# Kernel tuning notes

Hardware: AMD Instinct MI355X
Metric: run time of the kernel (lower is better)

Reference implementation:

```python
import jax, jax.numpy as jnp
import numpy as np

GRAPH_BIAS_SCALE = 0.7
COMMITMENT_COST = 0.25
DECAY = 0.995
EPS = 1e-6

N_TOKENS = 32768
LATENT = 512
N_SYMBOLS = 8192
EMBED_DIM = 2 * LATENT


def setup_inputs() -> dict:
    key = jax.random.key(0)
    ks = jax.random.split(key, 6)
    return {
        "z_real": jax.random.normal(ks[0], (N_TOKENS, LATENT), jnp.float32),
        "z_imag": jax.random.normal(ks[1], (N_TOKENS, LATENT), jnp.float32),
        "prev_symbol_idx": jax.random.randint(ks[2], (N_TOKENS,), 0, N_SYMBOLS, jnp.int64),
        "codebook": jax.random.normal(ks[3], (N_SYMBOLS, EMBED_DIM), jnp.float32),
        "cluster_size": jax.random.uniform(ks[4], (N_SYMBOLS,), jnp.float32),
        "embed_avg": jax.random.normal(ks[5], (N_SYMBOLS, EMBED_DIM), jnp.float32),
        "adjacency": jax.random.normal(jax.random.fold_in(key, 7), (N_SYMBOLS, N_SYMBOLS), jnp.float32),
    }


def reference(z_real, z_imag, prev_symbol_idx, codebook, cluster_size, embed_avg, adjacency):
    n_symbols = codebook.shape[0]
    z_flat = jnp.concatenate([z_real, z_imag], axis=-1)  # [N, 2*latent]

    # squared-distance matrix via matmul expansion: [N, n_symbols]
    d = (jnp.sum(z_flat ** 2, axis=1, keepdims=True)
         + jnp.sum(codebook ** 2, axis=1)
         - 2.0 * z_flat @ codebook.T)

    # graph-adjacency prior bias (row gather + sigmoid)
    bias = GRAPH_BIAS_SCALE * jax.nn.sigmoid(adjacency[prev_symbol_idx])
    d = d - bias

    min_indices = jnp.argmin(d, axis=1)          # [N]
    z_q = codebook[min_indices]                  # gather, pre-EMA codebook

    # --- EMA codebook update (training mode), scatter via segment_sum ---
    ones = jnp.ones(min_indices.shape, jnp.float32)
    counts = jax.ops.segment_sum(ones, min_indices, num_segments=n_symbols)
    new_cluster_size = cluster_size * DECAY + counts * (1.0 - DECAY)
    embed_sum = jax.ops.segment_sum(jax.lax.stop_gradient(z_flat), min_indices,
                                    num_segments=n_symbols)
    new_embed_avg = embed_avg * DECAY + embed_sum * (1.0 - DECAY)
    n_total = jnp.sum(new_cluster_size)
    cs = (new_cluster_size + EPS) / (n_total + n_symbols * EPS) * n_total
    new_codebook = new_embed_avg / cs[:, None]

    # --- losses and straight-through estimator ---
    loss_vq = jnp.mean((z_q - jax.lax.stop_gradient(z_flat)) ** 2)
    loss_commit = jnp.mean((jax.lax.stop_gradient(z_q) - z_flat) ** 2)
    loss = loss_vq + COMMITMENT_COST * loss_commit

    z_q_st = z_flat + jax.lax.stop_gradient(z_q - z_flat)
    D = z_real.shape[-1]
    z_complex = jax.lax.complex(z_q_st[..., :D], z_q_st[..., D:])

    return z_complex, loss, min_indices, new_codebook, new_cluster_size, new_embed_avg
```

## Files before the change

kernel.cpp:

```cpp
#include <hip/hip_runtime.h>
#include <math.h>
#include <float.h>

#define M_TOK   32768
#define NSYM    8192
#define KDIM    1024
#define LAT     512

#define DECAY_F 0.995f
#define OMD_F   0.005f
#define GBS_F   0.7f
#define EPS_F   1e-6f
#define WIN_F   2.5f

typedef unsigned short u16;
typedef unsigned int   u32;
typedef short short8 __attribute__((ext_vector_type(8)));
typedef float f32x4  __attribute__((ext_vector_type(4)));

#define GLOAD_LDS16(g, l) \
    __builtin_amdgcn_global_load_lds((const __attribute__((address_space(1))) u32*)(g), \
                                     (__attribute__((address_space(3))) u32*)(l), 16, 0, 0)

__device__ __forceinline__ u16 f2bf(float f) {
    u32 u = __float_as_uint(f);
    return (u16)((u + 0x7FFF + ((u >> 16) & 1)) >> 16);
}

__global__ void k_convA(const float* __restrict__ zr, const float* __restrict__ zi,
                        u16* __restrict__ A) {
    size_t t = (size_t)blockIdx.x * 256 + threadIdx.x;
    size_t base = t * 8;
    int tok = (int)(base >> 10);
    int k0  = (int)(base & 1023);
    const float* src = (k0 < 512) ? zr + (size_t)tok * 512 + k0
                                  : zi + (size_t)tok * 512 + (k0 - 512);
    float4 f0 = *(const float4*)src;
    float4 f1 = *(const float4*)(src + 4);
    u32 q0 = f2bf(f0.x) | ((u32)f2bf(f0.y) << 16);
    u32 q1 = f2bf(f0.z) | ((u32)f2bf(f0.w) << 16);
    u32 q2 = f2bf(f1.x) | ((u32)f2bf(f1.y) << 16);
    u32 q3 = f2bf(f1.z) | ((u32)f2bf(f1.w) << 16);
    *(uint4*)&A[base] = make_uint4(q0, q1, q2, q3);
}

__global__ void k_convB(const float* __restrict__ cb, u16* __restrict__ B,
                        float* __restrict__ cnorm) {
    size_t t = (size_t)blockIdx.x * 256 + threadIdx.x;
    size_t base = t * 8;
    float4 f0 = *(const float4*)&cb[base];
    float4 f1 = *(const float4*)&cb[base + 4];
    u32 q0 = f2bf(f0.x) | ((u32)f2bf(f0.y) << 16);
    u32 q1 = f2bf(f0.z) | ((u32)f2bf(f0.w) << 16);
    u32 q2 = f2bf(f1.x) | ((u32)f2bf(f1.y) << 16);
    u32 q3 = f2bf(f1.z) | ((u32)f2bf(f1.w) << 16);
    *(uint4*)&B[base] = make_uint4(q0, q1, q2, q3);
    float nrm = f0.x * f0.x + f0.y * f0.y + f0.z * f0.z + f0.w * f0.w
              + f1.x * f1.x + f1.y * f1.y + f1.z * f1.z + f1.w * f1.w;
#pragma unroll
    for (int m = 32; m; m >>= 1) nrm += __shfl_xor(nrm, m, 64);
    __shared__ float part[4];
    int lane = threadIdx.x & 63, w = threadIdx.x >> 6;
    if (lane == 0) part[w] = nrm;
    __syncthreads();
    if (threadIdx.x == 0)   cnorm[blockIdx.x * 2]     = part[0] + part[1];
    if (threadIdx.x == 128) cnorm[blockIdx.x * 2 + 1] = part[2] + part[3];
}

__global__ __launch_bounds__(256, 4) void k_screen(
    const u16* __restrict__ Ah, const u16* __restrict__ Bh,
    const float* __restrict__ cnorm,
    float* __restrict__ candV, u16* __restrict__ candI)
{
    __shared__ __align__(16) unsigned char smA[16384];
    __shared__ __align__(16) unsigned char smB[16384];
    __shared__ float smv[128][2][2];
    __shared__ float smi[128][2];

    const int sblk = (blockIdx.x & 7) * 128 + (blockIdx.x >> 3);
    const int bx = sblk >> 2;
    const int by = sblk & 3;

    const int tid  = threadIdx.x;
    const int lane = tid & 63;
    const int w    = tid >> 6;
    const int wr   = w >> 1, wc = w & 1;
    const int row0 = bx * 128;
    const int sBase = w * 256;

    for (int cc = 0; cc < 16; ++cc) {
        const int chunk = by * 16 + cc;
        const int colBase = chunk * 128;

        f32x4 acc[4][4];
#pragma unroll
        for (int m = 0; m < 4; ++m)
#pragma unroll
            for (int n = 0; n < 4; ++n) acc[m][n] = (f32x4){0.f, 0.f, 0.f, 0.f};

        for (int ks = 0; ks < 16; ++ks) {
            const int kk0 = ks * 64;
            __syncthreads();
#pragma unroll
            for (int i = 0; i < 4; ++i) {
                int slot = sBase + i * 64 + lane;
                int r = slot >> 3;
                int c = (slot & 7) ^ (r & 7);
                const u16* ga = Ah + ((size_t)(row0 + r) * KDIM + kk0 + c * 8);
                GLOAD_LDS16(ga, smA + (size_t)(sBase + i * 64) * 16);
                const u16* gb = Bh + ((size_t)(colBase + r) * KDIM + kk0 + c * 8);
                GLOAD_LDS16(gb, smB + (size_t)(sBase + i * 64) * 16);
            }
            __syncthreads();
#pragma unroll
            for (int h = 0; h < 2; ++h) {
                short8 af[4], bfr[4];
#pragma unroll
                for (int m = 0; m < 4; ++m) {
                    int r = wr * 64 + m * 16 + (lane & 15);
                    int byte = r * 128 + h * 64 + (lane >> 4) * 16;
                    byte ^= (r & 7) << 4;
                    af[m] = *(const short8*)(smA + byte);
                }
#pragma unroll
                for (int n = 0; n < 4; ++n) {
                    int r = wc * 64 + n * 16 + (lane & 15);
                    int byte = r * 128 + h * 64 + (lane >> 4) * 16;
                    byte ^= (r & 7) << 4;
                    bfr[n] = *(const short8*)(smB + byte);
                }
#pragma unroll
                for (int m = 0; m < 4; ++m)
#pragma unroll
                    for (int n = 0; n < 4; ++n)
                        acc[m][n] = __builtin_amdgcn_mfma_f32_16x16x32_bf16(
                            af[m], bfr[n], acc[m][n], 0, 0, 0);
            }
        }

        float cn[4];
#pragma unroll
        for (int n = 0; n < 4; ++n)
            cn[n] = cnorm[colBase + wc * 64 + n * 16 + (lane & 15)];

#pragma unroll
        for (int m = 0; m < 4; ++m)
#pragma unroll
            for (int j = 0; j < 4; ++j) {
                int rowL = wr * 64 + m * 16 + (lane >> 4) * 4 + j;
                float v1 = INFINITY, v2 = INFINITY, i1v = 0.f;
#pragma unroll
                for (int n = 0; n < 4; ++n) {
                    float s = cn[n] - 2.0f * acc[m][n][j];
                    float ci = (float)(colBase + wc * 64 + n * 16 + (lane & 15));
                    if (s < v1) { v2 = v1; v1 = s; i1v = ci; }
                    else v2 = fminf(v2, s);
                }
#pragma unroll
                for (int msk = 1; msk < 16; msk <<= 1) {
                    float o1 = __shfl_xor(v1, msk, 16);
                    float oi = __shfl_xor(i1v, msk, 16);
                    float o2 = __shfl_xor(v2, msk, 16);
                    float n2 = fminf(fminf(v2, o2), fmaxf(v1, o1));
                    if (o1 < v1) { v1 = o1; i1v = oi; }
                    v2 = n2;
                }
                if ((lane & 15) == 0) {
                    smv[rowL][wc][0] = v1;  smv[rowL][wc][1] = v2;
                    smi[rowL][wc] = i1v;
                }
            }
        __syncthreads();
        {
            int half = tid >> 7;
            int row  = tid & 127;
            float v1 = smv[row][half][0], v2 = smv[row][half][1];
            float iv = smi[row][half];
            size_t tcol = (size_t)(row0 + row);
            int halfIdx = chunk * 2 + half;
            candV[(size_t)(halfIdx * 2 + 0) * M_TOK + tcol] = v1;
            candV[(size_t)(halfIdx * 2 + 1) * M_TOK + tcol] = v2;
            candI[(size_t)halfIdx * M_TOK + tcol]           = (u16)iv;
        }
    }
}

__global__ void k_zero(u32* __restrict__ counts, u32* __restrict__ cursors,
                       u32* __restrict__ qcount, float* __restrict__ out_loss) {
    int i = blockIdx.x * 256 + threadIdx.x;
    if (i < NSYM) { counts[i] = 0; cursors[i] = 0; }
    if (i == 0) { out_loss[0] = 0.0f; qcount[0] = 0; }
}

__device__ __forceinline__ void rescore(
    const float* __restrict__ codebook, const float* __restrict__ adjacency,
    const double* zreg, int prw, int col, int lane, double& bestS, int& bestI)
{
    const float* crow = codebook + (size_t)col * KDIM;
    double dot = 0.0, cn2 = 0.0;
#pragma unroll
    for (int j = 0; j < 16; ++j) {
        double c = (double)crow[lane + 64 * j];
        dot += c * zreg[j]; cn2 += c * c;
    }
#pragma unroll
    for (int m = 32; m; m >>= 1) {
        dot += __shfl_xor(dot, m, 64);
        cn2 += __shfl_xor(cn2, m, 64);
    }
    double a = (double)adjacency[(size_t)prw * NSYM + col];
    double sc = cn2 - 2.0 * dot - (double)GBS_F / (1.0 + exp(-a));
    if (sc < bestS || (sc == bestS && col < bestI)) { bestS = sc; bestI = col; }
}

#define SEL_TOK 32
__global__ __launch_bounds__(256) void k_select(
    const float* __restrict__ zr, const float* __restrict__ zi,
    const int* __restrict__ prev,
    const float* __restrict__ codebook,
    const float* __restrict__ adjacency,
    const float* __restrict__ candV, const u16* __restrict__ candI,
    float* __restrict__ out_idx, u32* __restrict__ counts,
    u32* __restrict__ qcount, u32* __restrict__ queue)
{
    __shared__ float sv[256][SEL_TOK + 1];
    __shared__ u16   si[128][SEL_TOK + 2];
    const int tok0 = blockIdx.x * SEL_TOK;
    const int w = threadIdx.x >> 6, lane = threadIdx.x & 63;

    for (int idx = threadIdx.x; idx < 256 * SEL_TOK; idx += 256) {
        int e = idx >> 5, t = idx & (SEL_TOK - 1);
        sv[e][t] = candV[(size_t)e * M_TOK + tok0 + t];
    }
    for (int idx = threadIdx.x; idx < 128 * SEL_TOK; idx += 256) {
        int e = idx >> 5, t = idx & (SEL_TOK - 1);
        si[e][t] = candI[(size_t)e * M_TOK + tok0 + t];
    }
    __syncthreads();

    for (int tt = 0; tt < SEL_TOK / 4; ++tt) {
        const int t = w * (SEL_TOK / 4) + tt;
        const int tok = tok0 + t;
        float va1 = sv[4 * lane + 0][t];
        float va2 = sv[4 * lane + 1][t];
        float vb1 = sv[4 * lane + 2][t];
        float vb2 = sv[4 * lane + 3][t];
        int   ia  = (int)si[2 * lane + 0][t];
        int   ib  = (int)si[2 * lane + 1][t];

        float mm = fminf(va1, vb1);
#pragma unroll
        for (int m = 32; m; m >>= 1) mm = fminf(mm, __shfl_xor(mm, m, 64));
        const float thr = mm + WIN_F;

        unsigned long long m1a = __ballot(va1 <= thr);
        unsigned long long m1b = __ballot(vb1 <= thr);
        unsigned long long mh  = __ballot(va2 <= thr) | __ballot(vb2 <= thr);

        if (mh != 0) {
            if (lane == 0) { u32 q = atomicAdd(qcount, 1u); queue[q] = (u32)tok; }
        } else if (__popcll(m1a) + __popcll(m1b) == 1) {
            int bestI;
            if (m1a) { int c = __ffsll(m1a) - 1; bestI = __shfl(ia, c, 64); }
            else     { int c = __ffsll(m1b) - 1; bestI = __shfl(ib, c, 64); }
            if (lane == 0) {
                out_idx[tok] = (float)bestI;
                atomicAdd(&counts[bestI], 1u);
            }
        } else {
            double zreg[16];
#pragma unroll
            for (int j = 0; j < 8; ++j)
                zreg[j] = (double)zr[(size_t)tok * LAT + lane + 64 * j];
#pragma unroll
            for (int j = 0; j < 8; ++j)
                zreg[8 + j] = (double)zi[(size_t)tok * LAT + lane + 64 * j];
            const int prw = prev[tok];
            double bestS = DBL_MAX; int bestI = 0x7FFFFFFF;
            unsigned long long sa = m1a, sb = m1b;
            while (sa) { int c = __ffsll(sa) - 1; sa &= sa - 1;
                rescore(codebook, adjacency, zreg, prw, __shfl(ia, c, 64), lane, bestS, bestI); }
            while (sb) { int c = __ffsll(sb) - 1; sb &= sb - 1;
                rescore(codebook, adjacency, zreg, prw, __shfl(ib, c, 64), lane, bestS, bestI); }
            if (lane == 0) {
                out_idx[tok] = (float)bestI;
                atomicAdd(&counts[bestI], 1u);
            }
        }
    }
}

#define MAXC 384
__global__ __launch_bounds__(256) void k_rescan(
    const float* __restrict__ zr, const float* __restrict__ zi,
    const int* __restrict__ prev,
    const float* __restrict__ codebook,
    const float* __restrict__ adjacency,
    const float* __restrict__ candV, const u16* __restrict__ candI,
    const u32* __restrict__ qcount, const u32* __restrict__ queue,
    float* __restrict__ out_idx, u32* __restrict__ counts)
{
    __shared__ double zd[KDIM];
    __shared__ float v1h[128], v2h[128];
    __shared__ u16   i1h[128];
    __shared__ int   collist[MAXC];
    __shared__ int   nsing_sh, nh_sh, scanall_sh;
    __shared__ int   halves[128];
    __shared__ double wsc[4];
    __shared__ int    wix[4];
    __shared__ float  mm_sh;

    const int tid = threadIdx.x;
    const int w = tid >> 6, lane = tid & 63;
    const u32 nq = qcount[0];

    for (u32 qi = blockIdx.x; qi < nq; qi += gridDim.x) {
        const int tok = (int)queue[qi];

        if (tid < 128) {
            v1h[tid] = candV[(size_t)(tid * 2 + 0) * M_TOK + tok];
            v2h[tid] = candV[(size_t)(tid * 2 + 1) * M_TOK + tok];
            i1h[tid] = candI[(size_t)tid * M_TOK + tok];
        }
        for (int k = tid; k < LAT; k += 256) {
            zd[k]       = (double)zr[(size_t)tok * LAT + k];
            zd[LAT + k] = (double)zi[(size_t)tok * LAT + k];
        }
        if (tid == 0) { nsing_sh = 0; nh_sh = 0; scanall_sh = 0; }
        __syncthreads();

        if (tid < 64) {
            float m = fminf(v1h[tid], v1h[tid + 64]);
#pragma unroll
            for (int s = 32; s; s >>= 1) m = fminf(m, __shfl_xor(m, s, 64));
            if (tid == 0) mm_sh = m;
        }
        __syncthreads();
        const float thr = mm_sh + WIN_F;

        if (tid < 128) {
            bool hs = (v2h[tid] <= thr);
            if (hs) { int p = atomicAdd(&nh_sh, 1); halves[p] = tid; }
            else if (v1h[tid] <= thr) { int p = atomicAdd(&nsing_sh, 1); collist[p] = (int)i1h[tid]; }
        }
        __syncthreads();
        int nsing = nsing_sh, nh = nh_sh;
        int nc = nsing + nh * 64;
        if (nc > MAXC) { if (tid == 0) scanall_sh = 1; }
        __syncthreads();
        if (!scanall_sh) {
            for (int h = 0; h < nh; ++h) {
                if (tid < 64) collist[nsing + h * 64 + tid] = halves[h] * 64 + tid;
            }
            nc = nsing + nh * 64;
        }
        __syncthreads();

        const int prw = prev[tok];
        double bestS = DBL_MAX; int bestI = 0x7FFFFFFF;
        const int total = scanall_sh ? NSYM : nc;
        for (int ci = w; ci < total; ci += 4) {
            int col = scanall_sh ? ci : collist[ci];
            const float* crow = codebook + (size_t)col * KDIM;
            double dot = 0.0, cn2 = 0.0;
#pragma unroll
            for (int j = 0; j < 16; ++j) {
                double c = (double)crow[lane + 64 * j];
                dot += c * zd[lane + 64 * j]; cn2 += c * c;
            }
#pragma unroll
            for (int s = 32; s; s >>= 1) {
                dot += __shfl_xor(dot, s, 64);
                cn2 += __shfl_xor(cn2, s, 64);
            }
            double a = (double)adjacency[(size_t)prw * NSYM + col];
            double sc = cn2 - 2.0 * dot - (double)GBS_F / (1.0 + exp(-a));
            if (sc < bestS || (sc == bestS && col < bestI)) { bestS = sc; bestI = col; }
        }
        if (lane == 0) { wsc[w] = bestS; wix[w] = bestI; }
        __syncthreads();
        if (tid == 0) {
            double bs = wsc[0]; int bi = wix[0];
#pragma unroll
            for (int q = 1; q < 4; ++q) {
                if (wsc[q] < bs || (wsc[q] == bs && wix[q] < bi)) { bs = wsc[q]; bi = wix[q]; }
            }
            out_idx[tok] = (float)bi;
            atomicAdd(&counts[bi], 1u);
        }
        __syncthreads();
    }
}

__global__ __launch_bounds__(1024) void k_scan(
    const u32* __restrict__ counts, const float* __restrict__ cs_old,
    float* __restrict__ out_cs, u32* __restrict__ offsets,
    float* __restrict__ scal)
{
    const int tid = threadIdx.x;
    const int lane = tid & 63, w = tid >> 6;
    const int base = tid * 8;
    u32 c[8], pre[8], T = 0;
#pragma unroll
    for (int q = 0; q < 8; ++q) { c[q] = counts[base + q]; pre[q] = T; T += c[q]; }
    u32 inc = T;
#pragma unroll
    for (int d = 1; d < 64; d <<= 1) {
        u32 v = __shfl_up(inc, d, 64);
        if (lane >= d) inc += v;
    }
    __shared__ u32 wt[16];
    if (lane == 63) wt[w] = inc;
    __syncthreads();
    if (tid < 16) {
        u32 v = wt[tid];
#pragma unroll
        for (int d = 1; d < 16; d <<= 1) {
            u32 o = __shfl_up(v, d, 16);
            if (tid >= d) v += o;
        }
        wt[tid] = v;
    }
    __syncthreads();
    u32 ex = (w ? wt[w - 1] : 0) + inc - T;
#pragma unroll
    for (int q = 0; q < 8; ++q) offsets[base + q] = ex + pre[q];

    float nt = 0.0f;
#pragma unroll
    for (int q = 0; q < 8; ++q) {
        float ncs = cs_old[base + q] * DECAY_F + OMD_F * (float)c[q];
        out_cs[base + q] = ncs;
        nt += ncs;
    }
#pragma unroll
    for (int m = 32; m; m >>= 1) nt += __shfl_xor(nt, m, 64);
    __shared__ float red[16];
    if (lane == 0) red[w] = nt;
    __syncthreads();
    if (tid == 0) {
        float s = 0.0f;
#pragma unroll
        for (int i = 0; i < 16; ++i) s += red[i];
        scal[0] = s;
        scal[1] = s + (float)NSYM * EPS_F;
    }
}

__global__ void k_place(const float* __restrict__ idxf, const u32* __restrict__ offsets,
                        u32* __restrict__ cursors, u32* __restrict__ list) {
    int t = blockIdx.x * 256 + threadIdx.x;
    int s = (int)idxf[t];
    u32 slot = atomicAdd(&cursors[s], 1u);
    list[offsets[s] + slot] = (u32)t;
}

__global__ __launch_bounds__(128) void k_emit_fused(
    const float* __restrict__ zr, const float* __restrict__ zi,
    const float* __restrict__ codebook, const float* __restrict__ embed_avg,
    const u32* __restrict__ counts, const u32* __restrict__ offsets,
    const u32* __restrict__ list, const float* __restrict__ out_cs,
    const float* __restrict__ scal,
    float* __restrict__ out_ea, float* __restrict__ out_cb,
    float* __restrict__ out_zc, float* __restrict__ out_loss, int interleaved)
{
    const int s = blockIdx.x;
    const u32 cnt = counts[s], off = offsets[s];
    const int j = threadIdx.x * 4;
    float4 cbr = *(const float4*)&codebook[(size_t)s * KDIM + j];
    float4 cbi = *(const float4*)&codebook[(size_t)s * KDIM + LAT + j];
    float ar0 = 0.f, ar1 = 0.f, ar2 = 0.f, ar3 = 0.f;
    float ai0 = 0.f, ai1 = 0.f, ai2 = 0.f, ai3 = 0.f;
    float lsum = 0.f;
    for (u32 n = 0; n < cnt; ++n) {
        int t = (int)list[off + n];
        float4 z0 = *(const float4*)&zr[(size_t)t * LAT + j];
        float4 z1 = *(const float4*)&zi[(size_t)t * LAT + j];
        ar0 += z0.x; ar1 += z0.y; ar2 += z0.z; ar3 += z0.w;
        ai0 += z1.x; ai1 += z1.y; ai2 += z1.z; ai3 += z1.w;
        if (interleaved) {
            float2* dst = (float2*)out_zc + (size_t)t * LAT + j;
            dst[0] = make_float2(cbr.x, cbi.x); dst[1] = make_float2(cbr.y, cbi.y);
            dst[2] = make_float2(cbr.z, cbi.z); dst[3] = make_float2(cbr.w, cbi.w);
        } else {
            *(float4*)&out_zc[(size_t)t * LAT + j] = cbr;
        }
        float d;
        d = cbr.x - z0.x; lsum += d * d;  d = cbr.y - z0.y; lsum += d * d;
        d = cbr.z - z0.z; lsum += d * d;  d = cbr.w - z0.w; lsum += d * d;
        d = cbi.x - z1.x; lsum += d * d;  d = cbi.y - z1.y; lsum += d * d;
        d = cbi.z - z1.z; lsum += d * d;  d = cbi.w - z1.w; lsum += d * d;
    }
    float4 ea0 = *(const float4*)&embed_avg[(size_t)s * KDIM + j];
    float4 ea1 = *(const float4*)&embed_avg[(size_t)s * KDIM + LAT + j];
    float4 ner = make_float4(ea0.x * DECAY_F + ar0 * OMD_F, ea0.y * DECAY_F + ar1 * OMD_F,
                             ea0.z * DECAY_F + ar2 * OMD_F, ea0.w * DECAY_F + ar3 * OMD_F);
    float4 nei = make_float4(ea1.x * DECAY_F + ai0 * OMD_F, ea1.y * DECAY_F + ai1 * OMD_F,
                             ea1.z * DECAY_F + ai2 * OMD_F, ea1.w * DECAY_F + ai3 * OMD_F);
    *(float4*)&out_ea[(size_t)s * KDIM + j]       = ner;
    *(float4*)&out_ea[(size_t)s * KDIM + LAT + j] = nei;
    float ntot = scal[0], denom = scal[1];
    float cs = (out_cs[s] + EPS_F) / denom * ntot;
    float inv = 1.0f / cs;
    *(float4*)&out_cb[(size_t)s * KDIM + j] =
        make_float4(ner.x * inv, ner.y * inv, ner.z * inv, ner.w * inv);
    *(float4*)&out_cb[(size_t)s * KDIM + LAT + j] =
        make_float4(nei.x * inv, nei.y * inv, nei.z * inv, nei.w * inv);
#pragma unroll
    for (int m = 32; m; m >>= 1) lsum += __shfl_xor(lsum, m, 64);
    __shared__ float red[2];
    int wv = threadIdx.x >> 6, lane = threadIdx.x & 63;
    if (lane == 0) red[wv] = lsum;
    __syncthreads();
    if (threadIdx.x == 0) atomicAdd(out_loss, red[0] + red[1]);
}

__global__ __launch_bounds__(256) void k_emit(
    const float* __restrict__ zr, const float* __restrict__ zi,
    const float* __restrict__ embed_avg,
    const u32* __restrict__ counts, const u32* __restrict__ offsets,
    const u32* __restrict__ list, const float* __restrict__ out_cs,
    const float* __restrict__ scal,
    float* __restrict__ out_ea, float* __restrict__ out_cb)
{
    const int s = blockIdx.x;
    const u32 cnt = counts[s], off = offsets[s];
    const int j = threadIdx.x * 4;
    float a0 = 0.f, a1 = 0.f, a2 = 0.f, a3 = 0.f;
    for (u32 n = 0; n < cnt; ++n) {
        int t = (int)list[off + n];
        const float* src = (j < 512) ? zr + (size_t)t * 512 + j
                                     : zi + (size_t)t * 512 + (j - 512);
        float4 v = *(const float4*)src;
        a0 += v.x; a1 += v.y; a2 += v.z; a3 += v.w;
    }
    float4 ea = *(const float4*)&embed_avg[(size_t)s * KDIM + j];
    float4 nea = make_float4(ea.x * DECAY_F + a0 * OMD_F,
                             ea.y * DECAY_F + a1 * OMD_F,
                             ea.z * DECAY_F + a2 * OMD_F,
                             ea.w * DECAY_F + a3 * OMD_F);
    *(float4*)&out_ea[(size_t)s * KDIM + j] = nea;
    float ntot = scal[0], denom = scal[1];
    float cs = (out_cs[s] + EPS_F) / denom * ntot;
    float inv = 1.0f / cs;
    *(float4*)&out_cb[(size_t)s * KDIM + j] =
        make_float4(nea.x * inv, nea.y * inv, nea.z * inv, nea.w * inv);
}

__global__ __launch_bounds__(256) void k_zq(
    const float* __restrict__ zr, const float* __restrict__ zi,
    const float* __restrict__ codebook, const float* __restrict__ idxf,
    float* __restrict__ out_zc, float* __restrict__ out_loss, int interleaved)
{
    const int w = threadIdx.x >> 6, lane = threadIdx.x & 63;
    const int tok = blockIdx.x * 4 + w;
    const int mi = (int)idxf[tok];
    const int j0 = lane * 8;
    float4 re0 = *(const float4*)&codebook[(size_t)mi * KDIM + j0];
    float4 re1 = *(const float4*)&codebook[(size_t)mi * KDIM + j0 + 4];
    float4 im0 = *(const float4*)&codebook[(size_t)mi * KDIM + LAT + j0];
    float4 im1 = *(const float4*)&codebook[(size_t)mi * KDIM + LAT + j0 + 4];
    float4 zr0 = *(const float4*)&zr[(size_t)tok * LAT + j0];
    float4 zr1 = *(const float4*)&zr[(size_t)tok * LAT + j0 + 4];
    float4 zi0 = *(const float4*)&zi[(size_t)tok * LAT + j0];
    float4 zi1 = *(const float4*)&zi[(size_t)tok * LAT + j0 + 4];
    if (interleaved) {
        float2* dst = (float2*)out_zc + (size_t)tok * LAT + j0;
        dst[0] = make_float2(re0.x, im0.x); dst[1] = make_float2(re0.y, im0.y);
        dst[2] = make_float2(re0.z, im0.z); dst[3] = make_float2(re0.w, im0.w);
        dst[4] = make_float2(re1.x, im1.x); dst[5] = make_float2(re1.y, im1.y);
        dst[6] = make_float2(re1.z, im1.z); dst[7] = make_float2(re1.w, im1.w);
    } else {
        *(float4*)&out_zc[(size_t)tok * LAT + j0]     = re0;
        *(float4*)&out_zc[(size_t)tok * LAT + j0 + 4] = re1;
    }
    float l = 0.f;
    l += (re0.x-zr0.x)*(re0.x-zr0.x) + (re0.y-zr0.y)*(re0.y-zr0.y)
       + (re0.z-zr0.z)*(re0.z-zr0.z) + (re0.w-zr0.w)*(re0.w-zr0.w);
    l += (re1.x-zr1.x)*(re1.x-zr1.x) + (re1.y-zr1.y)*(re1.y-zr1.y)
       + (re1.z-zr1.z)*(re1.z-zr1.z) + (re1.w-zr1.w)*(re1.w-zr1.w);
    l += (im0.x-zi0.x)*(im0.x-zi0.x) + (im0.y-zi0.y)*(im0.y-zi0.y)
       + (im0.z-zi0.z)*(im0.z-zi0.z) + (im0.w-zi0.w)*(im0.w-zi0.w);
    l += (im1.x-zi1.x)*(im1.x-zi1.x) + (im1.y-zi1.y)*(im1.y-zi1.y)
       + (im1.z-zi1.z)*(im1.z-zi1.z) + (im1.w-zi1.w)*(im1.w-zi1.w);
#pragma unroll
    for (int m = 32; m; m >>= 1) l += __shfl_xor(l, m, 64);
    if (lane == 0) atomicAdd(out_loss, l);
}

__global__ void k_fin(float* __restrict__ out_loss) {
    out_loss[0] = out_loss[0] * 1.25f / 33554432.0f;
}

extern "C" void kernel_launch(void* const* d_in, const int* in_sizes, int n_in,
                              void* d_out, int out_size, void* d_ws, size_t ws_size,
                              hipStream_t stream) {
    const float* z_real     = (const float*)d_in[0];
    const float* z_imag     = (const float*)d_in[1];
    const int*   prev_idx   = (const int*)d_in[2];
    const float* codebook   = (const float*)d_in[3];
    const float* cluster_sz = (const float*)d_in[4];
    const float* embed_avg  = (const float*)d_in[5];
    const float* adjacency  = (const float*)d_in[6];

    float* out = (float*)d_out;

    const size_t REST = 1 + (size_t)M_TOK + (size_t)NSYM * KDIM + NSYM
                      + (size_t)NSYM * KDIM;
    size_t zc_n = (size_t)out_size - REST;
    const size_t n_z = (size_t)M_TOK * LAT;
    int interleaved = (zc_n >= 2 * n_z) ? 1 : 0;

    float* out_zc   = out;
    float* out_loss = out + zc_n;
    float* out_idx  = out + zc_n + 1;
    float* out_cb   = out + zc_n + 1 + M_TOK;
    float* out_cs   = out_cb + (size_t)NSYM * KDIM;
    float* out_ea   = out_cs + NSYM;

    u16*   A_hi  = (u16*)out_zc;
    u16*   B_hi  = (u16*)out_cb;
    float* cnorm = out_cb + 4194304;
    float* candV = out_ea;
    u16*   candI = (u16*)(out_cb + 4202496);

    const size_t WS_NEED = (size_t)(NSYM * 3 + M_TOK * 2 + 8) * 4;
    int use_ws = (ws_size >= WS_NEED) ? 1 : 0;
    u32 *counts, *cursors, *offsets, *list, *qcount, *queue;
    float* scal;
    if (use_ws) {
        u32* wsp = (u32*)d_ws;
        counts  = wsp;             cursors = counts + NSYM;
        offsets = cursors + NSYM;  list    = offsets + NSYM;
        queue   = list + M_TOK;
        scal    = (float*)(queue + M_TOK);
        qcount  = (u32*)(scal + 2);
    } else {
        counts  = (u32*)out_zc;    cursors = counts + NSYM;
        offsets = cursors + NSYM;  list    = offsets + NSYM;
        scal    = (float*)(list + M_TOK);
        qcount  = (u32*)(scal + 2);
        queue   = qcount + 1;
    }

    if (use_ws)
        k_zero<<<32, 256, 0, stream>>>(counts, cursors, qcount, out_loss);
    k_convA<<<16384, 256, 0, stream>>>(z_real, z_imag, A_hi);
    k_convB<<<4096, 256, 0, stream>>>(codebook, B_hi, cnorm);
    k_screen<<<1024, 256, 0, stream>>>(A_hi, B_hi, cnorm, candV, candI);
    if (!use_ws)
        k_zero<<<32, 256, 0, stream>>>(counts, cursors, qcount, out_loss);
    k_select<<<M_TOK / SEL_TOK, 256, 0, stream>>>(z_real, z_imag, prev_idx,
                                                  codebook, adjacency,
                                                  candV, candI, out_idx, counts,
                                                  qcount, queue);
    k_rescan<<<1024, 256, 0, stream>>>(z_real, z_imag, prev_idx, codebook,
                                       adjacency, candV, candI,
                                       qcount, queue, out_idx, counts);
    k_scan<<<1, 1024, 0, stream>>>(counts, cluster_sz, out_cs, offsets, scal);
    k_place<<<M_TOK / 256, 256, 0, stream>>>(out_idx, offsets, cursors, list);
    if (use_ws) {
        k_emit_fused<<<NSYM, 128, 0, stream>>>(z_real, z_imag, codebook, embed_avg,
                                               counts, offsets, list, out_cs, scal,
                                               out_ea, out_cb, out_zc, out_loss,
                                               interleaved);
    } else {
        k_emit<<<NSYM, 256, 0, stream>>>(z_real, z_imag, embed_avg, counts, offsets,
                                         list, out_cs, scal, out_ea, out_cb);
        k_zq<<<M_TOK / 4, 256, 0, stream>>>(z_real, z_imag, codebook, out_idx,
                                            out_zc, out_loss, interleaved);
    }
    k_fin<<<1, 1, 0, stream>>>(out_loss);
}
```

Measured before the change: 1.248 ms.

## Merge conversion and zeroing kernels, fuse scan with placement, drop final loss kernel

Merges the two bf16 conversion kernels and the zeroing kernel into one launch. Fuses the prefix scan with token placement in a single block that uses LDS atomics instead of global cursors, and folds the loss scaling into the atomic adds so the final one-thread kernel goes away. It also halves the tokens per select block and reduces the rescan grid. The aim is fewer launches and less global atomic traffic, at the cost of serialising 32K placements inside one workgroup.

```diff
diff --git a/kernel.cpp b/kernel.cpp
--- a/kernel.cpp
+++ b/kernel.cpp
@@ -12,6 +12,7 @@
 #define GBS_F   0.7f
 #define EPS_F   1e-6f
 #define WIN_F   2.5f
+#define LOSS_SCALE (1.25f / 33554432.0f)
 
 typedef unsigned short u16;
 typedef unsigned int   u32;
@@ -27,44 +28,53 @@
     return (u16)((u + 0x7FFF + ((u >> 16) & 1)) >> 16);
 }
 
-__global__ void k_convA(const float* __restrict__ zr, const float* __restrict__ zi,
-                        u16* __restrict__ A) {
-    size_t t = (size_t)blockIdx.x * 256 + threadIdx.x;
-    size_t base = t * 8;
-    int tok = (int)(base >> 10);
-    int k0  = (int)(base & 1023);
-    const float* src = (k0 < 512) ? zr + (size_t)tok * 512 + k0
-                                  : zi + (size_t)tok * 512 + (k0 - 512);
-    float4 f0 = *(const float4*)src;
-    float4 f1 = *(const float4*)(src + 4);
-    u32 q0 = f2bf(f0.x) | ((u32)f2bf(f0.y) << 16);
-    u32 q1 = f2bf(f0.z) | ((u32)f2bf(f0.w) << 16);
-    u32 q2 = f2bf(f1.x) | ((u32)f2bf(f1.y) << 16);
-    u32 q3 = f2bf(f1.z) | ((u32)f2bf(f1.w) << 16);
-    *(uint4*)&A[base] = make_uint4(q0, q1, q2, q3);
-}
-
-__global__ void k_convB(const float* __restrict__ cb, u16* __restrict__ B,
-                        float* __restrict__ cnorm) {
-    size_t t = (size_t)blockIdx.x * 256 + threadIdx.x;
-    size_t base = t * 8;
-    float4 f0 = *(const float4*)&cb[base];
-    float4 f1 = *(const float4*)&cb[base + 4];
-    u32 q0 = f2bf(f0.x) | ((u32)f2bf(f0.y) << 16);
-    u32 q1 = f2bf(f0.z) | ((u32)f2bf(f0.w) << 16);
-    u32 q2 = f2bf(f1.x) | ((u32)f2bf(f1.y) << 16);
-    u32 q3 = f2bf(f1.z) | ((u32)f2bf(f1.w) << 16);
-    *(uint4*)&B[base] = make_uint4(q0, q1, q2, q3);
-    float nrm = f0.x * f0.x + f0.y * f0.y + f0.z * f0.z + f0.w * f0.w
-              + f1.x * f1.x + f1.y * f1.y + f1.z * f1.z + f1.w * f1.w;
-#pragma unroll
-    for (int m = 32; m; m >>= 1) nrm += __shfl_xor(nrm, m, 64);
-    __shared__ float part[4];
-    int lane = threadIdx.x & 63, w = threadIdx.x >> 6;
-    if (lane == 0) part[w] = nrm;
-    __syncthreads();
-    if (threadIdx.x == 0)   cnorm[blockIdx.x * 2]     = part[0] + part[1];
-    if (threadIdx.x == 128) cnorm[blockIdx.x * 2 + 1] = part[2] + part[3];
+__global__ void k_conv(const float* __restrict__ zr, const float* __restrict__ zi,
+                       const float* __restrict__ cb,
+                       u16* __restrict__ A, u16* __restrict__ B,
+                       float* __restrict__ cnorm,
+                       u32* __restrict__ counts, u32* __restrict__ qcount,
+                       float* __restrict__ out_loss) {
+    const int bid = blockIdx.x;
+    if (bid < 16384) {
+        size_t t = (size_t)bid * 256 + threadIdx.x;
+        size_t base = t * 8;
+        int tok = (int)(base >> 10);
+        int k0  = (int)(base & 1023);
+        const float* src = (k0 < 512) ? zr + (size_t)tok * 512 + k0
+                                      : zi + (size_t)tok * 512 + (k0 - 512);
+        float4 f0 = *(const float4*)src;
+        float4 f1 = *(const float4*)(src + 4);
+        u32 q0 = f2bf(f0.x) | ((u32)f2bf(f0.y) << 16);
+        u32 q1 = f2bf(f0.z) | ((u32)f2bf(f0.w) << 16);
+        u32 q2 = f2bf(f1.x) | ((u32)f2bf(f1.y) << 16);
+        u32 q3 = f2bf(f1.z) | ((u32)f2bf(f1.w) << 16);
+        *(uint4*)&A[base] = make_uint4(q0, q1, q2, q3);
+    } else if (bid < 20480) {
+        const int b2 = bid - 16384;
+        size_t t = (size_t)b2 * 256 + threadIdx.x;
+        size_t base = t * 8;
+        float4 f0 = *(const float4*)&cb[base];
+        float4 f1 = *(const float4*)&cb[base + 4];
+        u32 q0 = f2bf(f0.x) | ((u32)f2bf(f0.y) << 16);
+        u32 q1 = f2bf(f0.z) | ((u32)f2bf(f0.w) << 16);
+        u32 q2 = f2bf(f1.x) | ((u32)f2bf(f1.y) << 16);
+        u32 q3 = f2bf(f1.z) | ((u32)f2bf(f1.w) << 16);
+        *(uint4*)&B[base] = make_uint4(q0, q1, q2, q3);
+        float nrm = f0.x * f0.x + f0.y * f0.y + f0.z * f0.z + f0.w * f0.w
+                  + f1.x * f1.x + f1.y * f1.y + f1.z * f1.z + f1.w * f1.w;
+#pragma unroll
+        for (int m = 32; m; m >>= 1) nrm += __shfl_xor(nrm, m, 64);
+        __shared__ float part[4];
+        int lane = threadIdx.x & 63, w = threadIdx.x >> 6;
+        if (lane == 0) part[w] = nrm;
+        __syncthreads();
+        if (threadIdx.x == 0)   cnorm[b2 * 2]     = part[0] + part[1];
+        if (threadIdx.x == 128) cnorm[b2 * 2 + 1] = part[2] + part[3];
+    } else {
+        int i = (bid - 20480) * 256 + threadIdx.x;
+        if (i < NSYM) counts[i] = 0;
+        if (i == 0) { qcount[0] = 0; out_loss[0] = 0.0f; }
+    }
 }
 
 __global__ __launch_bounds__(256, 4) void k_screen(
@@ -185,10 +195,10 @@
     }
 }
 
-__global__ void k_zero(u32* __restrict__ counts, u32* __restrict__ cursors,
-                       u32* __restrict__ qcount, float* __restrict__ out_loss) {
+__global__ void k_zero(u32* __restrict__ counts, u32* __restrict__ qcount,
+                       float* __restrict__ out_loss) {
     int i = blockIdx.x * 256 + threadIdx.x;
-    if (i < NSYM) { counts[i] = 0; cursors[i] = 0; }
+    if (i < NSYM) counts[i] = 0;
     if (i == 0) { out_loss[0] = 0.0f; qcount[0] = 0; }
 }
 
@@ -213,7 +223,7 @@
     if (sc < bestS || (sc == bestS && col < bestI)) { bestS = sc; bestI = col; }
 }
 
-#define SEL_TOK 32
+#define SEL_TOK 16
 __global__ __launch_bounds__(256) void k_select(
     const float* __restrict__ zr, const float* __restrict__ zi,
     const int* __restrict__ prev,
@@ -229,11 +239,11 @@
     const int w = threadIdx.x >> 6, lane = threadIdx.x & 63;
 
     for (int idx = threadIdx.x; idx < 256 * SEL_TOK; idx += 256) {
-        int e = idx >> 5, t = idx & (SEL_TOK - 1);
+        int e = idx >> 4, t = idx & (SEL_TOK - 1);
         sv[e][t] = candV[(size_t)e * M_TOK + tok0 + t];
     }
     for (int idx = threadIdx.x; idx < 128 * SEL_TOK; idx += 256) {
-        int e = idx >> 5, t = idx & (SEL_TOK - 1);
+        int e = idx >> 4, t = idx & (SEL_TOK - 1);
         si[e][t] = candI[(size_t)e * M_TOK + tok0 + t];
     }
     __syncthreads();
@@ -392,11 +402,15 @@
     }
 }
 
-__global__ __launch_bounds__(1024) void k_scan(
+__global__ __launch_bounds__(1024) void k_scanplace(
     const u32* __restrict__ counts, const float* __restrict__ cs_old,
+    const float* __restrict__ idxf,
     float* __restrict__ out_cs, u32* __restrict__ offsets,
-    float* __restrict__ scal)
-{
+    float* __restrict__ scal, u32* __restrict__ list)
+{
+    __shared__ u32 cur[NSYM];
+    __shared__ u32 wt[16];
+    __shared__ float red[16];
     const int tid = threadIdx.x;
     const int lane = tid & 63, w = tid >> 6;
     const int base = tid * 8;
@@ -409,7 +423,6 @@
         u32 v = __shfl_up(inc, d, 64);
         if (lane >= d) inc += v;
     }
-    __shared__ u32 wt[16];
     if (lane == 63) wt[w] = inc;
     __syncthreads();
     if (tid < 16) {
@@ -424,7 +437,10 @@
     __syncthreads();
     u32 ex = (w ? wt[w - 1] : 0) + inc - T;
 #pragma unroll
-    for (int q = 0; q < 8; ++q) offsets[base + q] = ex + pre[q];
+    for (int q = 0; q < 8; ++q) {
+        offsets[base + q] = ex + pre[q];
+        cur[base + q]     = ex + pre[q];
+    }
 
     float nt = 0.0f;
 #pragma unroll
@@ -435,7 +451,6 @@
     }
 #pragma unroll
     for (int m = 32; m; m >>= 1) nt += __shfl_xor(nt, m, 64);
-    __shared__ float red[16];
     if (lane == 0) red[w] = nt;
     __syncthreads();
     if (tid == 0) {
@@ -445,14 +460,13 @@
         scal[0] = s;
         scal[1] = s + (float)NSYM * EPS_F;
     }
-}
-
-__global__ void k_place(const float* __restrict__ idxf, const u32* __restrict__ offsets,
-                        u32* __restrict__ cursors, u32* __restrict__ list) {
-    int t = blockIdx.x * 256 + threadIdx.x;
-    int s = (int)idxf[t];
-    u32 slot = atomicAdd(&cursors[s], 1u);
-    list[offsets[s] + slot] = (u32)t;
+    __syncthreads();
+
+    for (int t = tid; t < M_TOK; t += 1024) {
+        int s = (int)idxf[t];
+        u32 slot = atomicAdd(&cur[s], 1u);
+        list[slot] = (u32)t;
+    }
 }
 
 __global__ __launch_bounds__(128) void k_emit_fused(
@@ -512,7 +526,7 @@
     int wv = threadIdx.x >> 6, lane = threadIdx.x & 63;
     if (lane == 0) red[wv] = lsum;
     __syncthreads();
-    if (threadIdx.x == 0) atomicAdd(out_loss, red[0] + red[1]);
+    if (threadIdx.x == 0) atomicAdd(out_loss, (red[0] + red[1]) * LOSS_SCALE);
 }
 
 __global__ __launch_bounds__(256) void k_emit(
@@ -585,11 +599,7 @@
        + (im1.z-zi1.z)*(im1.z-zi1.z) + (im1.w-zi1.w)*(im1.w-zi1.w);
 #pragma unroll
     for (int m = 32; m; m >>= 1) l += __shfl_xor(l, m, 64);
-    if (lane == 0) atomicAdd(out_loss, l);
-}
-
-__global__ void k_fin(float* __restrict__ out_loss) {
-    out_loss[0] = out_loss[0] * 1.25f / 33554432.0f;
+    if (lane == 0) atomicAdd(out_loss, l * LOSS_SCALE);
 }
 
 extern "C" void kernel_launch(void* const* d_in, const int* in_sizes, int n_in,
@@ -624,41 +634,39 @@
     float* candV = out_ea;
     u16*   candI = (u16*)(out_cb + 4202496);
 
-    const size_t WS_NEED = (size_t)(NSYM * 3 + M_TOK * 2 + 8) * 4;
+    const size_t WS_NEED = (size_t)(NSYM * 2 + M_TOK * 2 + 8) * 4;
     int use_ws = (ws_size >= WS_NEED) ? 1 : 0;
-    u32 *counts, *cursors, *offsets, *list, *qcount, *queue;
+    u32 *counts, *offsets, *list, *qcount, *queue;
     float* scal;
     if (use_ws) {
         u32* wsp = (u32*)d_ws;
-        counts  = wsp;             cursors = counts + NSYM;
-        offsets = cursors + NSYM;  list    = offsets + NSYM;
-        queue   = list + M_TOK;
+        counts  = wsp;             offsets = counts + NSYM;
+        list    = offsets + NSYM;  queue   = list + M_TOK;
         scal    = (float*)(queue + M_TOK);
         qcount  = (u32*)(scal + 2);
     } else {
-        counts  = (u32*)out_zc;    cursors = counts + NSYM;
-        offsets = cursors + NSYM;  list    = offsets + NSYM;
+        counts  = (u32*)out_zc;    offsets = counts + NSYM;
+        list    = offsets + NSYM;
         scal    = (float*)(list + M_TOK);
         qcount  = (u32*)(scal + 2);
         queue   = qcount + 1;
     }
 
-    if (use_ws)
-        k_zero<<<32, 256, 0, stream>>>(counts, cursors, qcount, out_loss);
-    k_convA<<<16384, 256, 0, stream>>>(z_real, z_imag, A_hi);
-    k_convB<<<4096, 256, 0, stream>>>(codebook, B_hi, cnorm);
+    k_conv<<<use_ws ? 20512 : 20480, 256, 0, stream>>>(z_real, z_imag, codebook,
+                                                       A_hi, B_hi, cnorm,
+                                                       counts, qcount, out_loss);
     k_screen<<<1024, 256, 0, stream>>>(A_hi, B_hi, cnorm, candV, candI);
     if (!use_ws)
-        k_zero<<<32, 256, 0, stream>>>(counts, cursors, qcount, out_loss);
+        k_zero<<<32, 256, 0, stream>>>(counts, qcount, out_loss);
     k_select<<<M_TOK / SEL_TOK, 256, 0, stream>>>(z_real, z_imag, prev_idx,
                                                   codebook, adjacency,
                                                   candV, candI, out_idx, counts,
                                                   qcount, queue);
-    k_rescan<<<1024, 256, 0, stream>>>(z_real, z_imag, prev_idx, codebook,
-                                       adjacency, candV, candI,
-                                       qcount, queue, out_idx, counts);
-    k_scan<<<1, 1024, 0, stream>>>(counts, cluster_sz, out_cs, offsets, scal);
-    k_place<<<M_TOK / 256, 256, 0, stream>>>(out_idx, offsets, cursors, list);
+    k_rescan<<<256, 256, 0, stream>>>(z_real, z_imag, prev_idx, codebook,
+                                      adjacency, candV, candI,
+                                      qcount, queue, out_idx, counts);
+    k_scanplace<<<1, 1024, 0, stream>>>(counts, cluster_sz, out_idx,
+                                        out_cs, offsets, scal, list);
     if (use_ws) {
         k_emit_fused<<<NSYM, 128, 0, stream>>>(z_real, z_imag, codebook, embed_avg,
                                                counts, offsets, list, out_cs, scal,
@@ -670,5 +678,4 @@
         k_zq<<<M_TOK / 4, 256, 0, stream>>>(z_real, z_imag, codebook, out_idx,
                                             out_zc, out_loss, interleaved);
     }
-    k_fin<<<1, 1, 0, stream>>>(out_loss);
-}
+}
```

Result: slower. 1.290 ms (+3.3%).

## Merge conversion and zeroing kernels, drop final loss kernel, widen EMA emit blocks

Applied to the files above, without the earlier changes.

Merges the A and B bf16 conversion kernels and the workspace zeroing into a single launch. The loss normalisation is folded into the per-block atomic adds, so the single-thread finalize kernel goes away. The fused EMA emit kernel now uses 256 threads, with two groups splitting each symbol's token list and combining partial sums through shared memory. The rescan grid shrinks from 1024 to 256 blocks, and the screening GEMM is split into two half-grid launches using a block offset. The aim is to cut launch overhead and add parallelism in the emit stage, at the cost of an extra launch for the screen and more float rounding in the loss from per-block scaling.

```diff
diff --git a/kernel.cpp b/kernel.cpp
--- a/kernel.cpp
+++ b/kernel.cpp
@@ -12,6 +12,7 @@
 #define GBS_F   0.7f
 #define EPS_F   1e-6f
 #define WIN_F   2.5f
+#define LOSS_SCALE (1.25f / 33554432.0f)
 
 typedef unsigned short u16;
 typedef unsigned int   u32;
@@ -27,57 +28,67 @@
     return (u16)((u + 0x7FFF + ((u >> 16) & 1)) >> 16);
 }
 
-__global__ void k_convA(const float* __restrict__ zr, const float* __restrict__ zi,
-                        u16* __restrict__ A) {
-    size_t t = (size_t)blockIdx.x * 256 + threadIdx.x;
-    size_t base = t * 8;
-    int tok = (int)(base >> 10);
-    int k0  = (int)(base & 1023);
-    const float* src = (k0 < 512) ? zr + (size_t)tok * 512 + k0
-                                  : zi + (size_t)tok * 512 + (k0 - 512);
-    float4 f0 = *(const float4*)src;
-    float4 f1 = *(const float4*)(src + 4);
-    u32 q0 = f2bf(f0.x) | ((u32)f2bf(f0.y) << 16);
-    u32 q1 = f2bf(f0.z) | ((u32)f2bf(f0.w) << 16);
-    u32 q2 = f2bf(f1.x) | ((u32)f2bf(f1.y) << 16);
-    u32 q3 = f2bf(f1.z) | ((u32)f2bf(f1.w) << 16);
-    *(uint4*)&A[base] = make_uint4(q0, q1, q2, q3);
-}
-
-__global__ void k_convB(const float* __restrict__ cb, u16* __restrict__ B,
-                        float* __restrict__ cnorm) {
-    size_t t = (size_t)blockIdx.x * 256 + threadIdx.x;
-    size_t base = t * 8;
-    float4 f0 = *(const float4*)&cb[base];
-    float4 f1 = *(const float4*)&cb[base + 4];
-    u32 q0 = f2bf(f0.x) | ((u32)f2bf(f0.y) << 16);
-    u32 q1 = f2bf(f0.z) | ((u32)f2bf(f0.w) << 16);
-    u32 q2 = f2bf(f1.x) | ((u32)f2bf(f1.y) << 16);
-    u32 q3 = f2bf(f1.z) | ((u32)f2bf(f1.w) << 16);
-    *(uint4*)&B[base] = make_uint4(q0, q1, q2, q3);
-    float nrm = f0.x * f0.x + f0.y * f0.y + f0.z * f0.z + f0.w * f0.w
-              + f1.x * f1.x + f1.y * f1.y + f1.z * f1.z + f1.w * f1.w;
-#pragma unroll
-    for (int m = 32; m; m >>= 1) nrm += __shfl_xor(nrm, m, 64);
-    __shared__ float part[4];
-    int lane = threadIdx.x & 63, w = threadIdx.x >> 6;
-    if (lane == 0) part[w] = nrm;
-    __syncthreads();
-    if (threadIdx.x == 0)   cnorm[blockIdx.x * 2]     = part[0] + part[1];
-    if (threadIdx.x == 128) cnorm[blockIdx.x * 2 + 1] = part[2] + part[3];
+__global__ void k_conv(const float* __restrict__ zr, const float* __restrict__ zi,
+                       const float* __restrict__ cb,
+                       u16* __restrict__ A, u16* __restrict__ B,
+                       float* __restrict__ cnorm,
+                       u32* __restrict__ counts, u32* __restrict__ cursors,
+                       u32* __restrict__ qcount, float* __restrict__ out_loss) {
+    const int bid = blockIdx.x;
+    if (bid < 16384) {
+        size_t t = (size_t)bid * 256 + threadIdx.x;
+        size_t base = t * 8;
+        int tok = (int)(base >> 10);
+        int k0  = (int)(base & 1023);
+        const float* src = (k0 < 512) ? zr + (size_t)tok * 512 + k0
+                                      : zi + (size_t)tok * 512 + (k0 - 512);
+        float4 f0 = *(const float4*)src;
+        float4 f1 = *(const float4*)(src + 4);
+        u32 q0 = f2bf(f0.x) | ((u32)f2bf(f0.y) << 16);
+        u32 q1 = f2bf(f0.z) | ((u32)f2bf(f0.w) << 16);
+        u32 q2 = f2bf(f1.x) | ((u32)f2bf(f1.y) << 16);
+        u32 q3 = f2bf(f1.z) | ((u32)f2bf(f1.w) << 16);
+        *(uint4*)&A[base] = make_uint4(q0, q1, q2, q3);
+    } else if (bid < 20480) {
+        const int b2 = bid - 16384;
+        size_t t = (size_t)b2 * 256 + threadIdx.x;
+        size_t base = t * 8;
+        float4 f0 = *(const float4*)&cb[base];
+        float4 f1 = *(const float4*)&cb[base + 4];
+        u32 q0 = f2bf(f0.x) | ((u32)f2bf(f0.y) << 16);
+        u32 q1 = f2bf(f0.z) | ((u32)f2bf(f0.w) << 16);
+        u32 q2 = f2bf(f1.x) | ((u32)f2bf(f1.y) << 16);
+        u32 q3 = f2bf(f1.z) | ((u32)f2bf(f1.w) << 16);
+        *(uint4*)&B[base] = make_uint4(q0, q1, q2, q3);
+        float nrm = f0.x * f0.x + f0.y * f0.y + f0.z * f0.z + f0.w * f0.w
+                  + f1.x * f1.x + f1.y * f1.y + f1.z * f1.z + f1.w * f1.w;
+#pragma unroll
+        for (int m = 32; m; m >>= 1) nrm += __shfl_xor(nrm, m, 64);
+        __shared__ float part[4];
+        int lane = threadIdx.x & 63, w = threadIdx.x >> 6;
+        if (lane == 0) part[w] = nrm;
+        __syncthreads();
+        if (threadIdx.x == 0)   cnorm[b2 * 2]     = part[0] + part[1];
+        if (threadIdx.x == 128) cnorm[b2 * 2 + 1] = part[2] + part[3];
+    } else {
+        int i = (bid - 20480) * 256 + threadIdx.x;
+        if (i < NSYM) { counts[i] = 0; cursors[i] = 0; }
+        if (i == 0) { qcount[0] = 0; out_loss[0] = 0.0f; }
+    }
 }
 
 __global__ __launch_bounds__(256, 4) void k_screen(
     const u16* __restrict__ Ah, const u16* __restrict__ Bh,
     const float* __restrict__ cnorm,
-    float* __restrict__ candV, u16* __restrict__ candI)
+    float* __restrict__ candV, u16* __restrict__ candI, int bofs)
 {
     __shared__ __align__(16) unsigned char smA[16384];
     __shared__ __align__(16) unsigned char smB[16384];
     __shared__ float smv[128][2][2];
     __shared__ float smi[128][2];
 
-    const int sblk = (blockIdx.x & 7) * 128 + (blockIdx.x >> 3);
+    const int gbid = blockIdx.x + bofs;
+    const int sblk = (gbid & 7) * 128 + (gbid >> 3);
     const int bx = sblk >> 2;
     const int by = sblk & 3;
 
@@ -455,7 +466,7 @@
     list[offsets[s] + slot] = (u32)t;
 }
 
-__global__ __launch_bounds__(128) void k_emit_fused(
+__global__ __launch_bounds__(256) void k_emit_fused(
     const float* __restrict__ zr, const float* __restrict__ zi,
     const float* __restrict__ codebook, const float* __restrict__ embed_avg,
     const u32* __restrict__ counts, const u32* __restrict__ offsets,
@@ -466,13 +477,14 @@
 {
     const int s = blockIdx.x;
     const u32 cnt = counts[s], off = offsets[s];
-    const int j = threadIdx.x * 4;
+    const int g = threadIdx.x >> 7;
+    const int j = (threadIdx.x & 127) * 4;
     float4 cbr = *(const float4*)&codebook[(size_t)s * KDIM + j];
     float4 cbi = *(const float4*)&codebook[(size_t)s * KDIM + LAT + j];
     float ar0 = 0.f, ar1 = 0.f, ar2 = 0.f, ar3 = 0.f;
     float ai0 = 0.f, ai1 = 0.f, ai2 = 0.f, ai3 = 0.f;
     float lsum = 0.f;
-    for (u32 n = 0; n < cnt; ++n) {
+    for (u32 n = g; n < cnt; n += 2) {
         int t = (int)list[off + n];
         float4 z0 = *(const float4*)&zr[(size_t)t * LAT + j];
         float4 z1 = *(const float4*)&zi[(size_t)t * LAT + j];
@@ -491,28 +503,41 @@
         d = cbi.x - z1.x; lsum += d * d;  d = cbi.y - z1.y; lsum += d * d;
         d = cbi.z - z1.z; lsum += d * d;  d = cbi.w - z1.w; lsum += d * d;
     }
-    float4 ea0 = *(const float4*)&embed_avg[(size_t)s * KDIM + j];
-    float4 ea1 = *(const float4*)&embed_avg[(size_t)s * KDIM + LAT + j];
-    float4 ner = make_float4(ea0.x * DECAY_F + ar0 * OMD_F, ea0.y * DECAY_F + ar1 * OMD_F,
-                             ea0.z * DECAY_F + ar2 * OMD_F, ea0.w * DECAY_F + ar3 * OMD_F);
-    float4 nei = make_float4(ea1.x * DECAY_F + ai0 * OMD_F, ea1.y * DECAY_F + ai1 * OMD_F,
-                             ea1.z * DECAY_F + ai2 * OMD_F, ea1.w * DECAY_F + ai3 * OMD_F);
-    *(float4*)&out_ea[(size_t)s * KDIM + j]       = ner;
-    *(float4*)&out_ea[(size_t)s * KDIM + LAT + j] = nei;
-    float ntot = scal[0], denom = scal[1];
-    float cs = (out_cs[s] + EPS_F) / denom * ntot;
-    float inv = 1.0f / cs;
-    *(float4*)&out_cb[(size_t)s * KDIM + j] =
-        make_float4(ner.x * inv, ner.y * inv, ner.z * inv, ner.w * inv);
-    *(float4*)&out_cb[(size_t)s * KDIM + LAT + j] =
-        make_float4(nei.x * inv, nei.y * inv, nei.z * inv, nei.w * inv);
+    __shared__ float comb[128][8];
+    if (g == 1) {
+        int r = threadIdx.x & 127;
+        comb[r][0] = ar0; comb[r][1] = ar1; comb[r][2] = ar2; comb[r][3] = ar3;
+        comb[r][4] = ai0; comb[r][5] = ai1; comb[r][6] = ai2; comb[r][7] = ai3;
+    }
+    __syncthreads();
+    if (g == 0) {
+        int r = threadIdx.x;
+        ar0 += comb[r][0]; ar1 += comb[r][1]; ar2 += comb[r][2]; ar3 += comb[r][3];
+        ai0 += comb[r][4]; ai1 += comb[r][5]; ai2 += comb[r][6]; ai3 += comb[r][7];
+        float4 ea0 = *(const float4*)&embed_avg[(size_t)s * KDIM + j];
+        float4 ea1 = *(const float4*)&embed_avg[(size_t)s * KDIM + LAT + j];
+        float4 ner = make_float4(ea0.x * DECAY_F + ar0 * OMD_F, ea0.y * DECAY_F + ar1 * OMD_F,
+                                 ea0.z * DECAY_F + ar2 * OMD_F, ea0.w * DECAY_F + ar3 * OMD_F);
+        float4 nei = make_float4(ea1.x * DECAY_F + ai0 * OMD_F, ea1.y * DECAY_F + ai1 * OMD_F,
+                                 ea1.z * DECAY_F + ai2 * OMD_F, ea1.w * DECAY_F + ai3 * OMD_F);
+        *(float4*)&out_ea[(size_t)s * KDIM + j]       = ner;
+        *(float4*)&out_ea[(size_t)s * KDIM + LAT + j] = nei;
+        float ntot = scal[0], denom = scal[1];
+        float cs = (out_cs[s] + EPS_F) / denom * ntot;
+        float inv = 1.0f / cs;
+        *(float4*)&out_cb[(size_t)s * KDIM + j] =
+            make_float4(ner.x * inv, ner.y * inv, ner.z * inv, ner.w * inv);
+        *(float4*)&out_cb[(size_t)s * KDIM + LAT + j] =
+            make_float4(nei.x * inv, nei.y * inv, nei.z * inv, nei.w * inv);
+    }
 #pragma unroll
     for (int m = 32; m; m >>= 1) lsum += __shfl_xor(lsum, m, 64);
-    __shared__ float red[2];
+    __shared__ float red[4];
     int wv = threadIdx.x >> 6, lane = threadIdx.x & 63;
     if (lane == 0) red[wv] = lsum;
     __syncthreads();
-    if (threadIdx.x == 0) atomicAdd(out_loss, red[0] + red[1]);
+    if (threadIdx.x == 0)
+        atomicAdd(out_loss, (red[0] + red[1] + red[2] + red[3]) * LOSS_SCALE);
 }
 
 __global__ __launch_bounds__(256) void k_emit(
@@ -585,11 +610,7 @@
        + (im1.z-zi1.z)*(im1.z-zi1.z) + (im1.w-zi1.w)*(im1.w-zi1.w);
 #pragma unroll
     for (int m = 32; m; m >>= 1) l += __shfl_xor(l, m, 64);
-    if (lane == 0) atomicAdd(out_loss, l);
-}
-
-__global__ void k_fin(float* __restrict__ out_loss) {
-    out_loss[0] = out_loss[0] * 1.25f / 33554432.0f;
+    if (lane == 0) atomicAdd(out_loss, l * LOSS_SCALE);
 }
 
 extern "C" void kernel_launch(void* const* d_in, const int* in_sizes, int n_in,
@@ -643,24 +664,25 @@
         queue   = qcount + 1;
     }
 
-    if (use_ws)
-        k_zero<<<32, 256, 0, stream>>>(counts, cursors, qcount, out_loss);
-    k_convA<<<16384, 256, 0, stream>>>(z_real, z_imag, A_hi);
-    k_convB<<<4096, 256, 0, stream>>>(codebook, B_hi, cnorm);
-    k_screen<<<1024, 256, 0, stream>>>(A_hi, B_hi, cnorm, candV, candI);
+    k_conv<<<use_ws ? 20512 : 20480, 256, 0, stream>>>(z_real, z_imag, codebook,
+                                                       A_hi, B_hi, cnorm,
+                                                       counts, cursors, qcount,
+                                                       out_loss);
+    k_screen<<<512, 256, 0, stream>>>(A_hi, B_hi, cnorm, candV, candI, 0);
+    k_screen<<<512, 256, 0, stream>>>(A_hi, B_hi, cnorm, candV, candI, 512);
     if (!use_ws)
         k_zero<<<32, 256, 0, stream>>>(counts, cursors, qcount, out_loss);
     k_select<<<M_TOK / SEL_TOK, 256, 0, stream>>>(z_real, z_imag, prev_idx,
                                                   codebook, adjacency,
                                                   candV, candI, out_idx, counts,
                                                   qcount, queue);
-    k_rescan<<<1024, 256, 0, stream>>>(z_real, z_imag, prev_idx, codebook,
-                                       adjacency, candV, candI,
-                                       qcount, queue, out_idx, counts);
+    k_rescan<<<256, 256, 0, stream>>>(z_real, z_imag, prev_idx, codebook,
+                                      adjacency, candV, candI,
+                                      qcount, queue, out_idx, counts);
     k_scan<<<1, 1024, 0, stream>>>(counts, cluster_sz, out_cs, offsets, scal);
     k_place<<<M_TOK / 256, 256, 0, stream>>>(out_idx, offsets, cursors, list);
     if (use_ws) {
-        k_emit_fused<<<NSYM, 128, 0, stream>>>(z_real, z_imag, codebook, embed_avg,
+        k_emit_fused<<<NSYM, 256, 0, stream>>>(z_real, z_imag, codebook, embed_avg,
                                                counts, offsets, list, out_cs, scal,
                                                out_ea, out_cb, out_zc, out_loss,
                                                interleaved);
@@ -670,5 +692,4 @@
         k_zq<<<M_TOK / 4, 256, 0, stream>>>(z_real, z_imag, codebook, out_idx,
                                             out_zc, out_loss, interleaved);
     }
-    k_fin<<<1, 1, 0, stream>>>(out_loss);
-}
+}
```

Result: slower. 1.378 ms (+10.4%).
